# Kernel optimization log

Measured on AMD Instinct MI355X. Metric: run time of the kernel, lower is better.

The kernel has to match this reference:

```python
import jax, jax.numpy as jnp
import numpy as np

NUM_EXPERTS = 64
TOP_K = 2
NOISE_EPS = 0.01


def setup_inputs() -> dict:
    key = jax.random.key(0)
    k1, k2, k3, k4 = jax.random.split(key, 4)
    B, D, E = 32768, 2048, NUM_EXPERTS
    x = jax.random.normal(k1, (B, D), dtype=jnp.float32)
    # original inits these to zero; use small random weights for a non-degenerate top-k
    w_gate = jax.random.normal(k2, (D, E), dtype=jnp.float32) * 0.02
    w_noise = jax.random.normal(k3, (D, E), dtype=jnp.float32) * 0.02
    noise = jax.random.normal(k4, (B, E), dtype=jnp.float32)  # tf.random.normal draw, fixed
    return {"x": x, "w_gate": w_gate, "w_noise": w_noise, "noise": noise}


def reference(x, w_gate, w_noise, noise):
    # routing_pooling='flatten' on a 2D input is identity
    pooled = x  # [B, D]
    routing = pooled @ w_gate  # [B, E]
    # noisy routing (training=True path)
    noise_stddev = jax.nn.softplus(pooled @ w_noise) + NOISE_EPS
    routing = routing + noise * noise_stddev
    # softmax_top_k: take top k+1, keep top k, softmax, scatter back to E experts
    kk = min(TOP_K + 1, NUM_EXPERTS)
    top_vals, top_idx = jax.lax.top_k(routing, kk)
    top_k_vals = top_vals[:, :TOP_K]            # [B, k]
    top_k_idx = top_idx[:, :TOP_K]              # [B, k]
    top_k_gates = jax.nn.softmax(top_k_vals, axis=-1)
    B = routing.shape[0]
    rows = jnp.arange(B)[:, None]
    # rowwise_unsorted_segment_sum -> scatter gates into expert slots
    out = jnp.zeros((B, NUM_EXPERTS), dtype=routing.dtype).at[rows, top_k_idx].add(top_k_gates)
    return out
```

## Files before the change

### kernel.cpp

```cpp
#include <hip/hip_runtime.h>
#include <math.h>


typedef _Float16 half4v __attribute__((ext_vector_type(4)));
typedef _Float16 half8v __attribute__((ext_vector_type(8)));
typedef float f32x4 __attribute__((ext_vector_type(4)));

constexpr int DIMK = 2048;
constexpr int NEXP = 64;
constexpr int BM   = 64;
constexpr int NCH  = DIMK / 32;

__device__ __forceinline__ void async_load16(const void* g, void* l) {
    __builtin_amdgcn_global_load_lds(
        (const __attribute__((address_space(1))) unsigned int*)g,
        (__attribute__((address_space(3))) unsigned int*)l, 16, 0, 0);
}

__device__ __forceinline__ bool gt_pair(float a, int ia, float b, int ib) {
    return (a > b) || (a == b && ia < ib);
}

__global__ __launch_bounds__(256)
void presplit_kernel(const float* __restrict__ wg, const float* __restrict__ wn,
                     _Float16* __restrict__ wsB)
{
    int gid  = blockIdx.x * 256 + threadIdx.x;
    int lane = gid & 63;
    int t    = (gid >> 6) & 7;
    int c    = gid >> 9;
    int n    = t * 16 + (lane & 15);
    int kb   = c * 32 + ((lane >> 4) << 3);
    const float* src = (n < NEXP) ? (wg + n) : (wn + (n - NEXP));
    half8v h1, h2;
    #pragma unroll
    for (int j = 0; j < 8; ++j) {
        float w = src[(size_t)(kb + j) * NEXP] * 65536.0f;
        _Float16 a = (_Float16)w;
        h1[j] = a;
        h2[j] = (_Float16)(w - (float)a);
    }
    *(half8v*)(wsB + ((((size_t)c * 2 + 0) * 8 + t) * 64 + lane) * 8) = h1;
    *(half8v*)(wsB + ((((size_t)c * 2 + 1) * 8 + t) * 64 + lane) * 8) = h2;
}

__global__ __launch_bounds__(256)
void routing_mfma(const float* __restrict__ x, const _Float16* __restrict__ wsB,
                  const float* __restrict__ noise, float* __restrict__ out)
{
    __shared__ float    Xs[2][BM][32];
    __shared__ _Float16 Bp[2][2][8][64][8];
    __shared__ _Float16 Ap[2][4][64][8];
    __shared__ float4   cand[BM][2];
    __shared__ float4   res[BM];

    const int tid  = threadIdx.x;
    const int lane = tid & 63;
    const int w    = tid >> 6;
    const int wm   = w >> 1;
    const int wnh  = w & 1;
    const int q    = lane >> 4;
    const int cidx = lane & 15;
    const int row0 = blockIdx.x * BM;

    f32x4 acc[2][4] = {};

    auto issue_loads = [&](int c, int buf) {
        #pragma unroll
        for (int ii = 0; ii < 2; ++ii) {
            int i = w * 2 + ii;
            const float* g = x + (size_t)(row0 + i * 8 + (lane >> 3)) * DIMK
                               + c * 32 + (lane & 7) * 4;
            async_load16(g, &Xs[buf][i * 8][0]);
        }
        #pragma unroll
        for (int ii = 0; ii < 4; ++ii) {
            int idx = w * 4 + ii;
            int p = idx >> 3, t = idx & 7;
            const _Float16* g = wsB + ((((size_t)c * 2 + p) * 8 + t) * 64 + lane) * 8;
            async_load16(g, &Bp[buf][p][t][0][0]);
        }
    };

    issue_loads(0, 0);

    for (int c = 0; c < NCH; ++c) {
        const int cur = c & 1;
        __syncthreads();
        if (c + 1 < NCH) issue_loads(c + 1, cur ^ 1);

        #pragma unroll
        for (int it = 0; it < 2; ++it) {
            int fidx = it * 1024 + tid * 4;
            int row  = fidx >> 5;
            int kk0  = fidx & 31;
            const float4 v = *(const float4*)(&Xs[cur][0][0] + fidx);
            float f0 = v.x * 1024.f, f1 = v.y * 1024.f;
            float f2 = v.z * 1024.f, f3 = v.w * 1024.f;
            half4v h1, h2;
            h1[0] = (_Float16)f0; h2[0] = (_Float16)(f0 - (float)h1[0]);
            h1[1] = (_Float16)f1; h2[1] = (_Float16)(f1 - (float)h1[1]);
            h1[2] = (_Float16)f2; h2[2] = (_Float16)(f2 - (float)h1[2]);
            h1[3] = (_Float16)f3; h2[3] = (_Float16)(f3 - (float)h1[3]);
            int mtile = row >> 4;
            int lp    = (row & 15) + ((kk0 >> 3) << 4);
            int j0    = kk0 & 7;
            *(half4v*)&Ap[0][mtile][lp][j0] = h1;
            *(half4v*)&Ap[1][mtile][lp][j0] = h2;
        }
        asm volatile("s_waitcnt lgkmcnt(0)\n\ts_barrier" ::: "memory");

        half8v af[2][2], bf[4][2];
        #pragma unroll
        for (int mt = 0; mt < 2; ++mt)
            #pragma unroll
            for (int p = 0; p < 2; ++p)
                af[mt][p] = *(const half8v*)&Ap[p][wm * 2 + mt][lane][0];
        #pragma unroll
        for (int tt = 0; tt < 4; ++tt) {
            int ntile = (tt < 2) ? (wnh * 2 + tt) : (4 + wnh * 2 + (tt - 2));
            #pragma unroll
            for (int p = 0; p < 2; ++p)
                bf[tt][p] = *(const half8v*)&Bp[cur][p][ntile][lane][0];
        }
        #pragma unroll
        for (int mt = 0; mt < 2; ++mt)
            #pragma unroll
            for (int tt = 0; tt < 4; ++tt) {
                acc[mt][tt] = __builtin_amdgcn_mfma_f32_16x16x32_f16(
                    af[mt][0], bf[tt][0], acc[mt][tt], 0, 0, 0);
                acc[mt][tt] = __builtin_amdgcn_mfma_f32_16x16x32_f16(
                    af[mt][0], bf[tt][1], acc[mt][tt], 0, 0, 0);
                acc[mt][tt] = __builtin_amdgcn_mfma_f32_16x16x32_f16(
                    af[mt][1], bf[tt][0], acc[mt][tt], 0, 0, 0);
            }
    }

    const float s = 0x1p-26f;
    #pragma unroll
    for (int mt = 0; mt < 2; ++mt) {
        float rv[2][4];
        #pragma unroll
        for (int g = 0; g < 2; ++g) {
            int e     = wnh * 32 + g * 16 + cidx;
            int rbase = row0 + wm * 32 + mt * 16 + q * 4;
            #pragma unroll
            for (int r = 0; r < 4; ++r) {
                float nz   = noise[(size_t)(rbase + r) * NEXP + e];
                float gate = acc[mt][g][r] * s;
                float nv   = acc[mt][g + 2][r] * s;
                float sp   = fmaxf(nv, 0.f) + log1pf(expf(-fabsf(nv)));
                rv[g][r]   = gate + nz * (sp + 0.01f);
            }
        }
        #pragma unroll
        for (int r = 0; r < 4; ++r) {
            int e0 = wnh * 32 + cidx, e1 = e0 + 16;
            float v1, v2; int i1, i2;
            float a = rv[0][r], b = rv[1][r];
            if (a >= b) { v1 = a; i1 = e0; v2 = b; i2 = e1; }
            else        { v1 = b; i1 = e1; v2 = a; i2 = e0; }
            #pragma unroll
            for (int m = 1; m <= 8; m <<= 1) {
                float b1 = __shfl_xor(v1, m); int ib1 = __shfl_xor(i1, m);
                float b2 = __shfl_xor(v2, m); int ib2 = __shfl_xor(i2, m);
                if (gt_pair(b1, ib1, v1, i1)) {
                    float o1 = v1; int oi1 = i1;
                    v1 = b1; i1 = ib1;
                    if (gt_pair(b2, ib2, o1, oi1)) { v2 = b2; i2 = ib2; }
                    else                           { v2 = o1; i2 = oi1; }
                } else if (gt_pair(b1, ib1, v2, i2)) {
                    v2 = b1; i2 = ib1;
                }
            }
            if (cidx == 0) {
                int rowb = wm * 32 + mt * 16 + q * 4 + r;
                cand[rowb][wnh] = make_float4(v1, __int_as_float(i1),
                                              v2, __int_as_float(i2));
            }
        }
    }
    __syncthreads();

    if (tid < BM) {
        float4 c0 = cand[tid][0], c1 = cand[tid][1];
        float mv1 = c0.x; int mi1 = __float_as_int(c0.y);
        float mv2 = c0.z; int mi2 = __float_as_int(c0.w);
        float b1 = c1.x;  int ib1 = __float_as_int(c1.y);
        float b2 = c1.z;  int ib2 = __float_as_int(c1.w);
        if (gt_pair(b1, ib1, mv1, mi1)) {
            float o1 = mv1; int oi1 = mi1;
            mv1 = b1; mi1 = ib1;
            if (gt_pair(b2, ib2, o1, oi1)) { mv2 = b2; mi2 = ib2; }
            else                           { mv2 = o1; mi2 = oi1; }
        } else if (gt_pair(b1, ib1, mv2, mi2)) {
            mv2 = b1; mi2 = ib1;
        }
        float t  = expf(mv2 - mv1);
        float g1 = 1.f / (1.f + t);
        res[tid] = make_float4(g1, __int_as_float(mi1),
                               t * g1, __int_as_float(mi2));
    }
    __syncthreads();

    {
        int rr  = tid >> 2;
        int seg = tid & 3;
        float4 rv = res[rr];
        float g1 = rv.x, g2 = rv.z;
        int   j1 = __float_as_int(rv.y), j2 = __float_as_int(rv.w);
        float* op = out + (size_t)(row0 + rr) * NEXP + seg * 16;
        #pragma unroll
        for (int qq = 0; qq < 4; ++qq) {
            int e0 = seg * 16 + qq * 4;
            float4 o;
            o.x = (e0 + 0 == j1) ? g1 : ((e0 + 0 == j2) ? g2 : 0.f);
            o.y = (e0 + 1 == j1) ? g1 : ((e0 + 1 == j2) ? g2 : 0.f);
            o.z = (e0 + 2 == j1) ? g1 : ((e0 + 2 == j2) ? g2 : 0.f);
            o.w = (e0 + 3 == j1) ? g1 : ((e0 + 3 == j2) ? g2 : 0.f);
            *(float4*)(op + qq * 4) = o;
        }
    }
}

extern "C" void kernel_launch(void* const* d_in, const int* in_sizes, int n_in,
                              void* d_out, int out_size, void* d_ws, size_t ws_size,
                              hipStream_t stream) {
    const float* x     = (const float*)d_in[0];
    const float* wg    = (const float*)d_in[1];
    const float* wn    = (const float*)d_in[2];
    const float* noise = (const float*)d_in[3];
    float* out = (float*)d_out;
    _Float16* wsB = (_Float16*)d_ws;

    presplit_kernel<<<dim3(128), 256, 0, stream>>>(wg, wn, wsB);

    const int Brows = in_sizes[0] / DIMK;
    dim3 grid(Brows / BM);
    routing_mfma<<<grid, 256, 0, stream>>>(x, wsB, noise, out);
}
```

Baseline: 422.6 us.

## Load A fragments directly into registers and deepen B LDS pipeline to four buffers

Removes the LDS staging of x (Xs and Ap buffers). Each lane now loads its own MFMA A fragment straight from global memory into registers, two chunks ahead, and does the fp16 hi/lo split in registers. The B weight buffer grows to four LDS stages with prefetch distance two, synchronized by explicit vmcnt waits and barriers. This aims to cut LDS traffic and one barrier per chunk, at the cost of more registers and less coalesced per-lane global loads of x.

Measured after the change: 419.3 us. Within noise of the previous version (-0.8%).

```diff
diff --git a/kernel.cpp b/kernel.cpp
--- a/kernel.cpp
+++ b/kernel.cpp
@@ -48,9 +48,7 @@
 void routing_mfma(const float* __restrict__ x, const _Float16* __restrict__ wsB,
                   const float* __restrict__ noise, float* __restrict__ out)
 {
-    __shared__ float    Xs[2][BM][32];
-    __shared__ _Float16 Bp[2][2][8][64][8];
-    __shared__ _Float16 Ap[2][4][64][8];
+    __shared__ _Float16 Bp[4][2][8][64][8];
     __shared__ float4   cand[BM][2];
     __shared__ float4   res[BM];
 
@@ -63,16 +61,13 @@
     const int cidx = lane & 15;
     const int row0 = blockIdx.x * BM;
 
-    f32x4 acc[2][4] = {};
-
-    auto issue_loads = [&](int c, int buf) {
-        #pragma unroll
-        for (int ii = 0; ii < 2; ++ii) {
-            int i = w * 2 + ii;
-            const float* g = x + (size_t)(row0 + i * 8 + (lane >> 3)) * DIMK
-                               + c * 32 + (lane & 7) * 4;
-            async_load16(g, &Xs[buf][i * 8][0]);
-        }
+    f32x4  acc[2][4] = {};
+    float4 ra[2][4];
+
+    const float* xr0 = x + (size_t)(row0 + wm * 32 + cidx) * DIMK + q * 8;
+    const float* xr1 = xr0 + 16 * DIMK;
+
+    auto issue_B = [&](int c, int buf) {
         #pragma unroll
         for (int ii = 0; ii < 4; ++ii) {
             int idx = w * 4 + ii;
@@ -82,59 +77,85 @@
         }
     };
 
-    issue_loads(0, 0);
-
-    for (int c = 0; c < NCH; ++c) {
-        const int cur = c & 1;
-        __syncthreads();
-        if (c + 1 < NCH) issue_loads(c + 1, cur ^ 1);
-
-        #pragma unroll
-        for (int it = 0; it < 2; ++it) {
-            int fidx = it * 1024 + tid * 4;
-            int row  = fidx >> 5;
-            int kk0  = fidx & 31;
-            const float4 v = *(const float4*)(&Xs[cur][0][0] + fidx);
-            float f0 = v.x * 1024.f, f1 = v.y * 1024.f;
-            float f2 = v.z * 1024.f, f3 = v.w * 1024.f;
-            half4v h1, h2;
-            h1[0] = (_Float16)f0; h2[0] = (_Float16)(f0 - (float)h1[0]);
-            h1[1] = (_Float16)f1; h2[1] = (_Float16)(f1 - (float)h1[1]);
-            h1[2] = (_Float16)f2; h2[2] = (_Float16)(f2 - (float)h1[2]);
-            h1[3] = (_Float16)f3; h2[3] = (_Float16)(f3 - (float)h1[3]);
-            int mtile = row >> 4;
-            int lp    = (row & 15) + ((kk0 >> 3) << 4);
-            int j0    = kk0 & 7;
-            *(half4v*)&Ap[0][mtile][lp][j0] = h1;
-            *(half4v*)&Ap[1][mtile][lp][j0] = h2;
-        }
-        asm volatile("s_waitcnt lgkmcnt(0)\n\ts_barrier" ::: "memory");
-
-        half8v af[2][2], bf[4][2];
-        #pragma unroll
-        for (int mt = 0; mt < 2; ++mt)
-            #pragma unroll
-            for (int p = 0; p < 2; ++p)
-                af[mt][p] = *(const half8v*)&Ap[p][wm * 2 + mt][lane][0];
-        #pragma unroll
-        for (int tt = 0; tt < 4; ++tt) {
-            int ntile = (tt < 2) ? (wnh * 2 + tt) : (4 + wnh * 2 + (tt - 2));
-            #pragma unroll
-            for (int p = 0; p < 2; ++p)
-                bf[tt][p] = *(const half8v*)&Bp[cur][p][ntile][lane][0];
-        }
-        #pragma unroll
-        for (int mt = 0; mt < 2; ++mt)
-            #pragma unroll
-            for (int tt = 0; tt < 4; ++tt) {
-                acc[mt][tt] = __builtin_amdgcn_mfma_f32_16x16x32_f16(
-                    af[mt][0], bf[tt][0], acc[mt][tt], 0, 0, 0);
-                acc[mt][tt] = __builtin_amdgcn_mfma_f32_16x16x32_f16(
-                    af[mt][0], bf[tt][1], acc[mt][tt], 0, 0, 0);
-                acc[mt][tt] = __builtin_amdgcn_mfma_f32_16x16x32_f16(
-                    af[mt][1], bf[tt][0], acc[mt][tt], 0, 0, 0);
-            }
-    }
+#define ISSUE_A(C, S)                                            \
+    {   const float* pa_ = xr0 + (C) * 32;                       \
+        const float* pb_ = xr1 + (C) * 32;                       \
+        ra[S][0] = *(const float4*)(pa_);                        \
+        ra[S][1] = *(const float4*)(pa_ + 4);                    \
+        ra[S][2] = *(const float4*)(pb_);                        \
+        ra[S][3] = *(const float4*)(pb_ + 4);  }
+
+#define FENCE() asm volatile("" ::: "memory")
+
+#define STEP(C, BUF, NBUF, SEL, ISS, WN)                                     \
+    {                                                                        \
+        asm volatile("s_waitcnt vmcnt(" #WN ")" ::: "memory");               \
+        asm volatile("s_barrier" ::: "memory");                              \
+        if (ISS) issue_B((C) + 2, NBUF);                                     \
+        half8v af[2][2];                                                     \
+        _Pragma("unroll")                                                    \
+        for (int mt = 0; mt < 2; ++mt) {                                     \
+            _Pragma("unroll")                                                \
+            for (int h = 0; h < 2; ++h) {                                    \
+                float4 v = ra[SEL][mt * 2 + h];                              \
+                float f0 = v.x * 1024.f, f1 = v.y * 1024.f;                  \
+                float f2 = v.z * 1024.f, f3 = v.w * 1024.f;                  \
+                _Float16 a0 = (_Float16)f0, a1 = (_Float16)f1;               \
+                _Float16 a2 = (_Float16)f2, a3 = (_Float16)f3;               \
+                af[mt][0][h * 4 + 0] = a0;                                   \
+                af[mt][0][h * 4 + 1] = a1;                                   \
+                af[mt][0][h * 4 + 2] = a2;                                   \
+                af[mt][0][h * 4 + 3] = a3;                                   \
+                af[mt][1][h * 4 + 0] = (_Float16)(f0 - (float)a0);           \
+                af[mt][1][h * 4 + 1] = (_Float16)(f1 - (float)a1);           \
+                af[mt][1][h * 4 + 2] = (_Float16)(f2 - (float)a2);           \
+                af[mt][1][h * 4 + 3] = (_Float16)(f3 - (float)a3);           \
+            }                                                                \
+        }                                                                    \
+        if (ISS) ISSUE_A((C) + 2, SEL);                                      \
+        half8v bf[4][2];                                                     \
+        _Pragma("unroll")                                                    \
+        for (int tt = 0; tt < 4; ++tt) {                                     \
+            int ntile = (tt < 2) ? (wnh * 2 + tt) : (4 + wnh * 2 + (tt - 2));\
+            _Pragma("unroll")                                                \
+            for (int p = 0; p < 2; ++p)                                      \
+                bf[tt][p] = *(const half8v*)&Bp[BUF][p][ntile][lane][0];     \
+        }                                                                    \
+        _Pragma("unroll")                                                    \
+        for (int mt = 0; mt < 2; ++mt) {                                     \
+            _Pragma("unroll")                                                \
+            for (int tt = 0; tt < 4; ++tt) {                                 \
+                acc[mt][tt] = __builtin_amdgcn_mfma_f32_16x16x32_f16(        \
+                    af[mt][0], bf[tt][0], acc[mt][tt], 0, 0, 0);             \
+                acc[mt][tt] = __builtin_amdgcn_mfma_f32_16x16x32_f16(        \
+                    af[mt][0], bf[tt][1], acc[mt][tt], 0, 0, 0);             \
+                acc[mt][tt] = __builtin_amdgcn_mfma_f32_16x16x32_f16(        \
+                    af[mt][1], bf[tt][0], acc[mt][tt], 0, 0, 0);             \
+            }                                                                \
+        }                                                                    \
+    }
+
+    issue_B(0, 0);
+    ISSUE_A(0, 0);
+    FENCE();
+    issue_B(1, 1);
+    ISSUE_A(1, 1);
+
+    #pragma unroll 1
+    for (int cb = 0; cb < NCH - 4; cb += 4) {
+        STEP(cb + 0, 0, 2, 0, 1, 8)
+        STEP(cb + 1, 1, 3, 1, 1, 8)
+        STEP(cb + 2, 2, 0, 0, 1, 8)
+        STEP(cb + 3, 3, 1, 1, 1, 8)
+    }
+    STEP(NCH - 4, 0, 2, 0, 1, 8)
+    STEP(NCH - 3, 1, 3, 1, 1, 8)
+    STEP(NCH - 2, 2, 0, 0, 0, 8)
+    STEP(NCH - 1, 3, 0, 1, 0, 0)
+
+#undef STEP
+#undef ISSUE_A
+#undef FENCE
 
     const float s = 0x1p-26f;
     #pragma unroll
```
